# Performance work log

Hardware: AMD Instinct MI355X
Metric: run time of the kernel (lower is better)

Reference implementation:

```python
import jax, jax.numpy as jnp
import numpy as np

D_MODEL = 1024
N_HEADS = 16
D_HEAD = D_MODEL // N_HEADS


def setup_inputs() -> dict:
    key = jax.random.key(0)
    ks = jax.random.split(key, 11)
    s = 0.02
    return {
        "X": jax.random.normal(ks[0], (4, 2048, D_MODEL), dtype=jnp.float32),
        "ln_gamma": jnp.ones((D_MODEL,), jnp.float32),
        "ln_beta": jnp.zeros((D_MODEL,), jnp.float32),
        "Wq": jax.random.normal(ks[1], (D_MODEL, D_MODEL), jnp.float32) * s,
        "bq": jnp.zeros((D_MODEL,), jnp.float32),
        "Wk": jax.random.normal(ks[2], (D_MODEL, D_MODEL), jnp.float32) * s,
        "bk": jnp.zeros((D_MODEL,), jnp.float32),
        "Wv": jax.random.normal(ks[3], (D_MODEL, D_MODEL), jnp.float32) * s,
        "bv": jnp.zeros((D_MODEL,), jnp.float32),
        "Wo": jax.random.normal(ks[4], (D_MODEL, D_MODEL), jnp.float32) * s,
        "bo": jnp.zeros((D_MODEL,), jnp.float32),
    }


def _attention(X, ln_gamma, ln_beta, Wq, bq, Wk, bk, Wv, bv, Wo, bo):
    B, S, D = X.shape
    H, Dh = N_HEADS, D_HEAD
    # LayerNorm over last dim
    mu = jnp.mean(X, axis=-1, keepdims=True)
    var = jnp.mean(jnp.square(X - mu), axis=-1, keepdims=True)
    Xn = (X - mu) * jax.lax.rsqrt(var + 1e-5) * ln_gamma + ln_beta
    # Projections (torch Linear: x @ W.T + b; W is [out, in])
    Q = (Xn @ Wq.T + bq).reshape(B, S, H, Dh).transpose(0, 2, 1, 3)
    K = (Xn @ Wk.T + bk).reshape(B, S, H, Dh).transpose(0, 2, 1, 3)
    V = (Xn @ Wv.T + bv).reshape(B, S, H, Dh).transpose(0, 2, 1, 3)
    scale = 1.0 / np.sqrt(Dh).astype(np.float32)
    scores = jnp.einsum("bhqd,bhkd->bhqk", Q * scale, K)  # [B,H,S,S]
    # p_dropout = 0.0 -> dropout is identity (applied before mask in original)
    # additive causal mask: 0 where q >= k, -inf otherwise
    causal = jnp.tril(jnp.ones((S, S), jnp.bool_))
    scores = jnp.where(causal, scores, -jnp.inf)
    A = jax.nn.softmax(scores, axis=-1)
    AV = jnp.einsum("bhqk,bhkd->bhqd", A, V)
    merged = AV.transpose(0, 2, 1, 3).reshape(B, S, D)
    return merged @ Wo.T + bo


def reference(X, ln_gamma, ln_beta, Wq, bq, Wk, bk, Wv, bv, Wo, bo):
    return _attention(X, ln_gamma, ln_beta, Wq, bq, Wk, bk, Wv, bv, Wo, bo)
```

## Files before the change

### kernel.cpp

```cpp
#include <hip/hip_runtime.h>

#define D_MODEL 1024
#define N_HEADS 16
#define D_HEAD 64
#define BATCH 4
#define SEQ 2048
#define TOKENS (BATCH * SEQ)
#define D_QKV 3072

#define QBLK 64
#define KBLK 64

typedef __attribute__((ext_vector_type(8))) short short8;
typedef __attribute__((ext_vector_type(4))) float f32x4;

__device__ __forceinline__ unsigned short f2bf(float f) {
    unsigned u = __float_as_uint(f);
    u += 0x7fffu + ((u >> 16) & 1u);
    return (unsigned short)(u >> 16);
}
__device__ __forceinline__ void gload16(const unsigned short* g, unsigned short* lds) {
    __builtin_amdgcn_global_load_lds((const __attribute__((address_space(1))) void*)g,
                                     (__attribute__((address_space(3))) void*)lds, 16, 0, 0);
}

__global__ void ln_kernel(const float* __restrict__ X, const float* __restrict__ gamma,
                          const float* __restrict__ beta, unsigned short* __restrict__ Xn) {
    const int t = blockIdx.x;
    const int tid = threadIdx.x;
    const float4 v = ((const float4*)(X + (size_t)t * D_MODEL))[tid];
    float s  = v.x + v.y + v.z + v.w;
    float s2 = v.x * v.x + v.y * v.y + v.z * v.z + v.w * v.w;
    for (int off = 32; off > 0; off >>= 1) {
        s  += __shfl_xor(s,  off);
        s2 += __shfl_xor(s2, off);
    }
    __shared__ float sh[8];
    const int wv = tid >> 6;
    if ((tid & 63) == 0) { sh[wv] = s; sh[4 + wv] = s2; }
    __syncthreads();
    const float ts  = sh[0] + sh[1] + sh[2] + sh[3];
    const float ts2 = sh[4] + sh[5] + sh[6] + sh[7];
    const float mu  = ts * (1.0f / D_MODEL);
    const float var = ts2 * (1.0f / D_MODEL) - mu * mu;
    const float rs  = rsqrtf(var + 1e-5f);
    const float4 gm = ((const float4*)gamma)[tid];
    const float4 bt = ((const float4*)beta)[tid];
    ushort4 o;
    o.x = f2bf((v.x - mu) * rs * gm.x + bt.x);
    o.y = f2bf((v.y - mu) * rs * gm.y + bt.y);
    o.z = f2bf((v.z - mu) * rs * gm.z + bt.z);
    o.w = f2bf((v.w - mu) * rs * gm.w + bt.w);
    ((ushort4*)Xn)[(size_t)t * (D_MODEL / 4) + tid] = o;
}

__global__ void cvt_all(const float* __restrict__ Wq, const float* __restrict__ Wk,
                        const float* __restrict__ Wv, const float* __restrict__ Wo,
                        unsigned short* __restrict__ Wqkv, unsigned short* __restrict__ WoB) {
    const int i = blockIdx.x * blockDim.x + threadIdx.x;
    const int mtx  = i >> 18;
    const int elem = i & 262143;
    const float* src;
    unsigned short* dst;
    if (mtx == 0)      { src = Wq; dst = Wqkv; }
    else if (mtx == 1) { src = Wk; dst = Wqkv + (1 << 20); }
    else if (mtx == 2) { src = Wv; dst = Wqkv + (2 << 20); }
    else               { src = Wo; dst = WoB; }
    const float4 v = ((const float4*)src)[elem];
    ushort4 o;
    o.x = f2bf(v.x); o.y = f2bf(v.y); o.z = f2bf(v.z); o.w = f2bf(v.w);
    ((ushort4*)dst)[elem] = o;
}

__global__ void transpose_v(const unsigned short* __restrict__ QKV, unsigned short* __restrict__ out) {
    __shared__ __attribute__((aligned(16))) unsigned short T[64][72];
    const int tid = threadIdx.x;
    const int s0 = blockIdx.x * 64;
    const int n0 = blockIdx.y * 64;
    const int b  = blockIdx.z;
    const int r = tid >> 2, c = (tid & 3) * 16;
    const unsigned short* ip = QKV + ((size_t)(b * SEQ + s0 + r)) * D_QKV + 2048 + n0 + c;
    *(short8*)&T[r][c]     = *(const short8*)ip;
    *(short8*)&T[r][c + 8] = *(const short8*)(ip + 8);
    __syncthreads();
    unsigned short* op = out + ((size_t)(b * D_MODEL + n0 + r)) * SEQ + s0 + c;
    short8 o0, o1;
    #pragma unroll
    for (int j = 0; j < 8; ++j) { o0[j] = (short)T[c + j][r]; o1[j] = (short)T[c + 8 + j][r]; }
    *(short8*)op       = o0;
    *(short8*)(op + 8) = o1;
}

template <bool OUT_BF16>
__global__ __launch_bounds__(256) void gemm128(const unsigned short* __restrict__ A,
                                               const unsigned short* __restrict__ B,
                                               const float* __restrict__ b0,
                                               const float* __restrict__ b1,
                                               const float* __restrict__ b2,
                                               void* __restrict__ out,
                                               int M, int N, int K, float qscale) {
    __shared__ __attribute__((aligned(16))) unsigned short As[2][128 * 64];
    __shared__ __attribute__((aligned(16))) unsigned short Bs[2][128 * 64];
    const int tid  = threadIdx.x;
    const int lane = tid & 63;
    const int w    = tid >> 6;
    const int wm = w >> 1, wn = w & 1;
    const int m0 = blockIdx.y * 128;
    const int n0 = blockIdx.x * 128;
    const int lr = lane & 15, lg = lane >> 4;

    const int crow  = lane >> 3;
    const int uslot = (lane & 7) ^ crow;

    const unsigned short* Ab = A + (size_t)m0 * K + uslot * 8;
    const unsigned short* Bb = B + (size_t)n0 * K + uslot * 8;

    #pragma unroll
    for (int i = 0; i < 4; ++i) {
        const int c = w * 4 + i;
        const int grow = c * 8 + crow;
        gload16(Ab + (size_t)grow * K, &As[0][c * 512]);
        gload16(Bb + (size_t)grow * K, &Bs[0][c * 512]);
    }
    __syncthreads();

    f32x4 acc[4][4] = {};
    const int NT = K >> 6;
    int cur = 0;
    for (int kt = 0; kt < NT; ++kt) {
        if (kt + 1 < NT) {
            const int k1 = (kt + 1) << 6;
            #pragma unroll
            for (int i = 0; i < 4; ++i) {
                const int c = w * 4 + i;
                const int grow = c * 8 + crow;
                gload16(Ab + (size_t)grow * K + k1, &As[cur ^ 1][c * 512]);
                gload16(Bb + (size_t)grow * K + k1, &Bs[cur ^ 1][c * 512]);
            }
        }
        #pragma unroll
        for (int h = 0; h < 2; ++h) {
            short8 af[4], bf[4];
            #pragma unroll
            for (int mi = 0; mi < 4; ++mi) {
                const int row = wm * 64 + mi * 16 + lr;
                const int slot = (h * 4 + lg) ^ (row & 7);
                af[mi] = *(const short8*)(&As[cur][row * 64 + slot * 8]);
            }
            #pragma unroll
            for (int ni = 0; ni < 4; ++ni) {
                const int row = wn * 64 + ni * 16 + lr;
                const int slot = (h * 4 + lg) ^ (row & 7);
                bf[ni] = *(const short8*)(&Bs[cur][row * 64 + slot * 8]);
            }
            #pragma unroll
            for (int mi = 0; mi < 4; ++mi)
                #pragma unroll
                for (int ni = 0; ni < 4; ++ni)
                    acc[mi][ni] = __builtin_amdgcn_mfma_f32_16x16x32_bf16(af[mi], bf[ni], acc[mi][ni], 0, 0, 0);
        }
        __syncthreads();
        cur ^= 1;
    }

    const int seg = blockIdx.x >> 3;
    const float* bp = (seg == 0) ? b0 : (seg == 1) ? b1 : b2;
    const float osc = (seg == 0) ? qscale : 1.0f;
    #pragma unroll
    for (int ni = 0; ni < 4; ++ni) {
        const int n = n0 + wn * 64 + ni * 16 + lr;
        const float bv = bp[n & 1023];
        #pragma unroll
        for (int mi = 0; mi < 4; ++mi) {
            const int mb = m0 + wm * 64 + mi * 16 + lg * 4;
            #pragma unroll
            for (int i = 0; i < 4; ++i) {
                const float val = (acc[mi][ni][i] + bv) * osc;
                if (OUT_BF16) ((unsigned short*)out)[(size_t)(mb + i) * N + n] = f2bf(val);
                else          ((float*)out)[(size_t)(mb + i) * N + n] = val;
            }
        }
    }
}

__global__ __launch_bounds__(256) void flash_attn(const unsigned short* __restrict__ QKV,
                                                  const unsigned short* __restrict__ Vt,
                                                  unsigned short* __restrict__ Mo) {
    __shared__ __attribute__((aligned(16))) unsigned short KtL[2][KBLK * 64];
    __shared__ __attribute__((aligned(16))) unsigned short VsL[2][64 * KBLK];
    __shared__ __attribute__((aligned(16))) unsigned short Pq[4 * 4 * 16 * 24];

    const int tid  = threadIdx.x;
    const int lane = tid & 63;
    const int w    = tid >> 6;
    const int F   = blockIdx.x;
    const int xcd = F & 7;
    const int r_  = F >> 3;
    const int qb  = 31 - (r_ & 31);
    const int bh  = xcd | ((r_ >> 5) << 3);
    const int b = bh >> 4, h = bh & 15;
    const int q0 = qb * QBLK;
    const int lg = lane >> 4;
    const int lr = lane & 15;

    const size_t tokbase = (size_t)b * SEQ;
    const size_t hoff = (size_t)h * D_HEAD;

    const int crow  = lane >> 3;
    const int uslot = (lane & 7) ^ crow;

    const short* Qp = (const short*)QKV + (tokbase + q0 + w * 16 + lr) * D_QKV + hoff + lg * 8;
    const short8 qf0 = *(const short8*)(Qp);
    const short8 qf1 = *(const short8*)(Qp + 32);

    const unsigned short* Kg = QKV + (tokbase) * D_QKV + 1024 + hoff + uslot * 8;
    const unsigned short* Vg = Vt + ((size_t)bh * 64) * SEQ + uslot * 8;

    int koff[2][4];
    #pragma unroll
    for (int hh = 0; hh < 2; ++hh)
        #pragma unroll
        for (int s4 = 0; s4 < 4; ++s4)
            koff[hh][s4] = (s4 * 16 + lr) * 64 + (((hh * 4 + lg) ^ (lr & 7)) * 8);
    const int pwbase = w * 1536 + lg * 96 + lr;
    int prd[2];
    #pragma unroll
    for (int c2 = 0; c2 < 2; ++c2)
        prd[c2] = w * 1536 + (c2 * 2 + (lg >> 1)) * 384 + lr * 24 + (lg & 1) * 8;

    float m[4], l[4];
    f32x4 acc[4];
    #pragma unroll
    for (int i = 0; i < 4; ++i) { m[i] = -INFINITY; l[i] = 0.f; acc[i] = (f32x4){0.f,0.f,0.f,0.f}; }

    const int ntiles = qb + 1;

    #pragma unroll
    for (int i = 0; i < 2; ++i) {
        const int c = w * 2 + i;
        const int row = c * 8 + crow;
        gload16(Kg + (size_t)row * D_QKV, &KtL[0][c * 512]);
        gload16(Vg + (size_t)row * SEQ, &VsL[0][c * 512]);
    }
    __syncthreads();

    int cur = 0;
    for (int t = 0; t < ntiles; ++t) {
        if (t + 1 < ntiles) {
            const int k1 = (t + 1) * KBLK;
            #pragma unroll
            for (int i = 0; i < 2; ++i) {
                const int c = w * 2 + i;
                const int row = c * 8 + crow;
                gload16(Kg + (size_t)(k1 + row) * D_QKV, &KtL[cur ^ 1][c * 512]);
                gload16(Vg + (size_t)row * SEQ + k1, &VsL[cur ^ 1][c * 512]);
            }
        }
        const unsigned short* Kc = KtL[cur];
        const unsigned short* Vc = VsL[cur];

        f32x4 sc[4];
        __builtin_amdgcn_s_setprio(1);
        #pragma unroll
        for (int s4 = 0; s4 < 4; ++s4) {
            const short8 kf0 = *(const short8*)(Kc + koff[0][s4]);
            const short8 kf1 = *(const short8*)(Kc + koff[1][s4]);
            f32x4 z = {0.f, 0.f, 0.f, 0.f};
            z = __builtin_amdgcn_mfma_f32_16x16x32_bf16(qf0, kf0, z, 0, 0, 0);
            z = __builtin_amdgcn_mfma_f32_16x16x32_bf16(qf1, kf1, z, 0, 0, 0);
            sc[s4] = z;
        }
        __builtin_amdgcn_s_setprio(0);

        if (t == qb) {
            const int qr = w * 16 + lg * 4;
            #pragma unroll
            for (int s4 = 0; s4 < 4; ++s4) {
                const int kk = s4 * 16 + lr;
                #pragma unroll
                for (int i = 0; i < 4; ++i)
                    sc[s4][i] = (kk <= qr + i) ? sc[s4][i] : -INFINITY;
            }
        }

        float rm[4];
        bool need = false;
        #pragma unroll
        for (int i = 0; i < 4; ++i) {
            float r = fmaxf(fmaxf(sc[0][i], sc[1][i]), fmaxf(sc[2][i], sc[3][i]));
            r = fmaxf(r, __shfl_xor(r, 1));
            r = fmaxf(r, __shfl_xor(r, 2));
            r = fmaxf(r, __shfl_xor(r, 4));
            r = fmaxf(r, __shfl_xor(r, 8));
            rm[i] = r;
            need |= (r > m[i] + 8.0f);
        }
        if (__any(need)) {
            #pragma unroll
            for (int i = 0; i < 4; ++i) {
                const float mn = fmaxf(m[i], rm[i]);
                const float c  = __builtin_exp2f(m[i] - mn);
                m[i] = mn;
                l[i] *= c;
                #pragma unroll
                for (int ds = 0; ds < 4; ++ds) acc[ds][i] *= c;
            }
        }

        #pragma unroll
        for (int i = 0; i < 4; ++i) {
            float rs = 0.f;
            #pragma unroll
            for (int s4 = 0; s4 < 4; ++s4) {
                const float p = __builtin_exp2f(sc[s4][i] - m[i]);
                sc[s4][i] = p;
                rs += p;
            }
            rs += __shfl_xor(rs, 1); rs += __shfl_xor(rs, 2);
            rs += __shfl_xor(rs, 4); rs += __shfl_xor(rs, 8);
            l[i] += rs;
        }
        #pragma unroll
        for (int s4 = 0; s4 < 4; ++s4)
            #pragma unroll
            for (int i = 0; i < 4; ++i) {
                const unsigned u = __float_as_uint(sc[s4][i]) + 0x8000u;
                Pq[pwbase + s4 * 384 + i * 24] = (unsigned short)(u >> 16);
            }

        __builtin_amdgcn_s_setprio(1);
        #pragma unroll
        for (int c2 = 0; c2 < 2; ++c2) {
            const short8 pf = *(const short8*)(Pq + prd[c2]);
            #pragma unroll
            for (int ds = 0; ds < 4; ++ds) {
                const short8 vf = *(const short8*)(Vc + koff[c2][ds]);
                acc[ds] = __builtin_amdgcn_mfma_f32_16x16x32_bf16(pf, vf, acc[ds], 0, 0, 0);
            }
        }
        __builtin_amdgcn_s_setprio(0);

        __syncthreads();
        cur ^= 1;
    }

    const int gq = q0 + w * 16 + lg * 4;
    #pragma unroll
    for (int ds = 0; ds < 4; ++ds) {
        #pragma unroll
        for (int i = 0; i < 4; ++i) {
            const float o = acc[ds][i] / l[i];
            Mo[(tokbase + gq + i) * D_MODEL + hoff + ds * 16 + lr] = f2bf(o);
        }
    }
}

extern "C" void kernel_launch(void* const* d_in, const int* in_sizes, int n_in,
                              void* d_out, int out_size, void* d_ws, size_t ws_size,
                              hipStream_t stream) {
    const float* X  = (const float*)d_in[0];
    const float* lg = (const float*)d_in[1];
    const float* lb = (const float*)d_in[2];
    const float* Wq = (const float*)d_in[3];
    const float* bq = (const float*)d_in[4];
    const float* Wk = (const float*)d_in[5];
    const float* bk = (const float*)d_in[6];
    const float* Wv = (const float*)d_in[7];
    const float* bv = (const float*)d_in[8];
    const float* Wo = (const float*)d_in[9];
    const float* bo = (const float*)d_in[10];
    float* out = (float*)d_out;

    char* ws = (char*)d_ws;
    const size_t MB = 1024 * 1024;
    unsigned short* Xn   = (unsigned short*)(ws + 0);
    unsigned short* Vtg  = (unsigned short*)(ws + 0);
    unsigned short* Wqkv = (unsigned short*)(ws + 16 * MB);
    unsigned short* WoB  = (unsigned short*)(ws + 22 * MB);
    unsigned short* QKVb = (unsigned short*)(ws + 24 * MB);
    unsigned short* Mb   = (unsigned short*)(ws + 72 * MB);

    ln_kernel<<<TOKENS, 256, 0, stream>>>(X, lg, lb, Xn);

    cvt_all<<<4096, 256, 0, stream>>>(Wq, Wk, Wv, Wo, Wqkv, WoB);

    const float qscale = 0.125f * 1.44269504088896f;
    dim3 qkvgrid(D_QKV / 128, TOKENS / 128);
    gemm128<true><<<qkvgrid, 256, 0, stream>>>(Xn, Wqkv, bq, bk, bv, QKVb,
                                               TOKENS, D_QKV, D_MODEL, qscale);

    dim3 tgrid(SEQ / 64, D_MODEL / 64, BATCH);
    transpose_v<<<tgrid, 256, 0, stream>>>(QKVb, Vtg);

    flash_attn<<<(SEQ / QBLK) * BATCH * N_HEADS, 256, 0, stream>>>(QKVb, Vtg, Mb);

    dim3 ogrid(D_MODEL / 128, TOKENS / 128);
    gemm128<false><<<ogrid, 256, 0, stream>>>(Mb, WoB, bo, bo, bo, out,
                                              TOKENS, D_MODEL, D_MODEL, 1.0f);
}
```

Baseline: 359.2 us.

## Compute transposed S tile so softmax reductions stay mostly in-lane

```diff
diff --git a/kernel.cpp b/kernel.cpp
--- a/kernel.cpp
+++ b/kernel.cpp
@@ -188,7 +188,7 @@
                                                   unsigned short* __restrict__ Mo) {
     __shared__ __attribute__((aligned(16))) unsigned short KtL[2][KBLK * 64];
     __shared__ __attribute__((aligned(16))) unsigned short VsL[2][64 * KBLK];
-    __shared__ __attribute__((aligned(16))) unsigned short Pq[4 * 4 * 16 * 24];
+    __shared__ __attribute__((aligned(16))) unsigned int   Pq[4 * 16 * 32];
 
     const int tid  = threadIdx.x;
     const int lane = tid & 63;
@@ -222,16 +222,20 @@
         #pragma unroll
         for (int s4 = 0; s4 < 4; ++s4)
             koff[hh][s4] = (s4 * 16 + lr) * 64 + (((hh * 4 + lg) ^ (lr & 7)) * 8);
-    const int pwbase = w * 1536 + lg * 96 + lr;
+
+    const int sxor = lr & 3;
+    const int pw   = w * 512 + lr * 32 + lg * 2;
     int prd[2];
     #pragma unroll
     for (int c2 = 0; c2 < 2; ++c2)
-        prd[c2] = w * 1536 + (c2 * 2 + (lg >> 1)) * 384 + lr * 24 + (lg & 1) * 8;
-
-    float m[4], l[4];
-    f32x4 acc[4];
-    #pragma unroll
-    for (int i = 0; i < 4; ++i) { m[i] = -INFINITY; l[i] = 0.f; acc[i] = (f32x4){0.f,0.f,0.f,0.f}; }
+        prd[c2] = w * 512 + lr * 32 + (lg & 1) * 4 + ((((c2 << 1) + (lg >> 1)) ^ sxor) << 3);
+
+    int qaddr[4];
+    #pragma unroll
+    for (int i = 0; i < 4; ++i) qaddr[i] = (lg * 4 + i) * 4;
+
+    float m = -INFINITY, l = 0.f;
+    f32x4 acc[4] = {};
 
     const int ntiles = qb + 1;
 
@@ -259,74 +263,71 @@
         const unsigned short* Kc = KtL[cur];
         const unsigned short* Vc = VsL[cur];
 
-        f32x4 sc[4];
+        f32x4 st[4];
         __builtin_amdgcn_s_setprio(1);
         #pragma unroll
         for (int s4 = 0; s4 < 4; ++s4) {
             const short8 kf0 = *(const short8*)(Kc + koff[0][s4]);
             const short8 kf1 = *(const short8*)(Kc + koff[1][s4]);
             f32x4 z = {0.f, 0.f, 0.f, 0.f};
-            z = __builtin_amdgcn_mfma_f32_16x16x32_bf16(qf0, kf0, z, 0, 0, 0);
-            z = __builtin_amdgcn_mfma_f32_16x16x32_bf16(qf1, kf1, z, 0, 0, 0);
-            sc[s4] = z;
+            z = __builtin_amdgcn_mfma_f32_16x16x32_bf16(kf0, qf0, z, 0, 0, 0);
+            z = __builtin_amdgcn_mfma_f32_16x16x32_bf16(kf1, qf1, z, 0, 0, 0);
+            st[s4] = z;
         }
         __builtin_amdgcn_s_setprio(0);
 
         if (t == qb) {
-            const int qr = w * 16 + lg * 4;
+            const int qloc = w * 16 + lr;
             #pragma unroll
             for (int s4 = 0; s4 < 4; ++s4) {
-                const int kk = s4 * 16 + lr;
+                const int kb = s4 * 16 + lg * 4;
                 #pragma unroll
-                for (int i = 0; i < 4; ++i)
-                    sc[s4][i] = (kk <= qr + i) ? sc[s4][i] : -INFINITY;
-            }
-        }
-
-        float rm[4];
-        bool need = false;
-        #pragma unroll
-        for (int i = 0; i < 4; ++i) {
-            float r = fmaxf(fmaxf(sc[0][i], sc[1][i]), fmaxf(sc[2][i], sc[3][i]));
-            r = fmaxf(r, __shfl_xor(r, 1));
-            r = fmaxf(r, __shfl_xor(r, 2));
-            r = fmaxf(r, __shfl_xor(r, 4));
-            r = fmaxf(r, __shfl_xor(r, 8));
-            rm[i] = r;
-            need |= (r > m[i] + 8.0f);
-        }
-        if (__any(need)) {
+                for (int r = 0; r < 4; ++r)
+                    st[s4][r] = (kb + r <= qloc) ? st[s4][r] : -INFINITY;
+            }
+        }
+
+        float pmax = st[0][0];
+        #pragma unroll
+        for (int s4 = 0; s4 < 4; ++s4)
+            #pragma unroll
+            for (int r = 0; r < 4; ++r) pmax = fmaxf(pmax, st[s4][r]);
+        pmax = fmaxf(pmax, __shfl_xor(pmax, 16));
+        pmax = fmaxf(pmax, __shfl_xor(pmax, 32));
+
+        if (__any(pmax > m + 8.0f)) {
+            const float mn = fmaxf(m, pmax);
+            const float c  = __builtin_exp2f(m - mn);
+            m = mn;
+            l *= c;
             #pragma unroll
             for (int i = 0; i < 4; ++i) {
-                const float mn = fmaxf(m[i], rm[i]);
-                const float c  = __builtin_exp2f(m[i] - mn);
-                m[i] = mn;
-                l[i] *= c;
+                const float cb = __uint_as_float(
+                    (unsigned)__builtin_amdgcn_ds_bpermute(qaddr[i], (int)__float_as_uint(c)));
                 #pragma unroll
-                for (int ds = 0; ds < 4; ++ds) acc[ds][i] *= c;
-            }
-        }
-
-        #pragma unroll
-        for (int i = 0; i < 4; ++i) {
-            float rs = 0.f;
-            #pragma unroll
-            for (int s4 = 0; s4 < 4; ++s4) {
-                const float p = __builtin_exp2f(sc[s4][i] - m[i]);
-                sc[s4][i] = p;
-                rs += p;
-            }
-            rs += __shfl_xor(rs, 1); rs += __shfl_xor(rs, 2);
-            rs += __shfl_xor(rs, 4); rs += __shfl_xor(rs, 8);
-            l[i] += rs;
-        }
-        #pragma unroll
-        for (int s4 = 0; s4 < 4; ++s4)
-            #pragma unroll
-            for (int i = 0; i < 4; ++i) {
-                const unsigned u = __float_as_uint(sc[s4][i]) + 0x8000u;
-                Pq[pwbase + s4 * 384 + i * 24] = (unsigned short)(u >> 16);
-            }
+                for (int ds = 0; ds < 4; ++ds) acc[ds][i] *= cb;
+            }
+        }
+
+        float rs = 0.f;
+        #pragma unroll
+        for (int s4 = 0; s4 < 4; ++s4) {
+            float p0 = __builtin_exp2f(st[s4][0] - m);
+            float p1 = __builtin_exp2f(st[s4][1] - m);
+            float p2 = __builtin_exp2f(st[s4][2] - m);
+            float p3 = __builtin_exp2f(st[s4][3] - m);
+            rs += (p0 + p1) + (p2 + p3);
+            const unsigned u0 = __float_as_uint(p0) + 0x8000u;
+            const unsigned u1 = __float_as_uint(p1) + 0x8000u;
+            const unsigned u2 = __float_as_uint(p2) + 0x8000u;
+            const unsigned u3 = __float_as_uint(p3) + 0x8000u;
+            const int pb = pw + (((s4 ^ sxor) << 3));
+            Pq[pb]     = (u1 & 0xffff0000u) | (u0 >> 16);
+            Pq[pb + 1] = (u3 & 0xffff0000u) | (u2 >> 16);
+        }
+        rs += __shfl_xor(rs, 16);
+        rs += __shfl_xor(rs, 32);
+        l += rs;
 
         __builtin_amdgcn_s_setprio(1);
         #pragma unroll
@@ -344,12 +345,18 @@
         cur ^= 1;
     }
 
+    const float linv = 1.0f / l;
+    float lb[4];
+    #pragma unroll
+    for (int i = 0; i < 4; ++i)
+        lb[i] = __uint_as_float(
+            (unsigned)__builtin_amdgcn_ds_bpermute(qaddr[i], (int)__float_as_uint(linv)));
     const int gq = q0 + w * 16 + lg * 4;
     #pragma unroll
     for (int ds = 0; ds < 4; ++ds) {
         #pragma unroll
         for (int i = 0; i < 4; ++i) {
-            const float o = acc[ds][i] / l[i];
+            const float o = acc[ds][i] * lb[i];
             Mo[(tokbase + gq + i) * D_MODEL + hoff + ds * 16 + lr] = f2bf(o);
         }
     }
```

New measurement: 310.8 us. 1.16x faster.
